# Optimization experiments

Hardware: AMD Instinct MI355X
Metric: run time of the kernel (lower is better)

Reference implementation:

```python
import jax, jax.numpy as jnp
import numpy as np


def _bilinear_warp(img, flow):
    """grid_sample(img, base_grid + flow), bilinear, zeros padding, align_corners=True.
    img: [N, C, H, W]; flow: [N, 2, H, W] with channels (dx, dy) in pixels."""
    N, C, H, W = img.shape
    ys, xs = jnp.meshgrid(jnp.arange(H, dtype=img.dtype),
                          jnp.arange(W, dtype=img.dtype), indexing='ij')
    x = xs[None] + flow[:, 0]  # [N, H, W] sample x-coord in pixels
    y = ys[None] + flow[:, 1]
    x0 = jnp.floor(x)
    y0 = jnp.floor(y)
    wx1 = x - x0
    wy1 = y - y0

    def tap(xi, yi, w):
        valid = (xi >= 0) & (xi <= W - 1) & (yi >= 0) & (yi <= H - 1)
        xc = jnp.clip(xi, 0, W - 1).astype(jnp.int32)
        yc = jnp.clip(yi, 0, H - 1).astype(jnp.int32)
        # per-image gather: im[:, yy, xx] -> [C, H, W]
        vals = jax.vmap(lambda im, yy, xx: im[:, yy, xx])(img, yc, xc)
        return vals * (w * valid.astype(img.dtype))[:, None]

    return (tap(x0,       y0,       (1.0 - wx1) * (1.0 - wy1)) +
            tap(x0 + 1.0, y0,       wx1         * (1.0 - wy1)) +
            tap(x0,       y0 + 1.0, (1.0 - wx1) * wy1) +
            tap(x0 + 1.0, y0 + 1.0, wx1         * wy1))


def _to_batch(t):
    # [B, C, T, H, W] -> cat(unbind(dim=2), dim=0) -> [T*B, C, H, W]
    B, C, T, H, W = t.shape
    return jnp.moveaxis(t, 2, 0).reshape(T * B, C, H, W)


def setup_inputs() -> dict:
    key = jax.random.key(0)
    k1, k2, k3, k4 = jax.random.split(key, 4)
    B, C, T, H, W = 8, 2, 8, 512, 512
    flow = jax.random.normal(k1, (B, C, T, H, W), dtype=jnp.float32) * 8.0
    flowback = jax.random.normal(k2, (B, C, T, H, W), dtype=jnp.float32) * 8.0
    mask_fw = jax.random.uniform(k3, (B, 1, T, H, W), dtype=jnp.float32)
    mask_bw = jax.random.uniform(k4, (B, 1, T, H, W), dtype=jnp.float32)
    return {"flow": flow, "flowback": flowback, "mask_fw": mask_fw,
            "mask_bw": mask_bw, "num_predicted_frames": 8}


def reference(flow, flowback, mask_fw, mask_bw, num_predicted_frames):
    f = _to_batch(flow)        # [T*B, 2, H, W]
    fb = _to_batch(flowback)
    mf = _to_batch(mask_fw)    # [T*B, 1, H, W]
    mb = _to_batch(mask_bw)
    nextloss = jnp.mean(mf * jnp.abs(_bilinear_warp(fb, f) + f))
    prevloss = jnp.mean(mb * jnp.abs(_bilinear_warp(f, fb) + fb))
    return (prevloss + nextloss) * num_predicted_frames
```

## Files before the change

### kernel.cpp

```cpp
#include <hip/hip_runtime.h>

#define BB 8
#define CC 2
#define TT 8
#define HH 512
#define WW 512
#define HWSZ (HH * WW)
#define TOTAL_ELEMS ((double)(BB * CC * TT) * (double)HWSZ)

__device__ __forceinline__ float2 ld2(const float* __restrict__ p) {
    float2 v;
    __builtin_memcpy(&v, p, sizeof(float2));
    return v;
}

__device__ __forceinline__ void bilin2(const float* __restrict__ c0,
                                       const float* __restrict__ c1,
                                       float sx, float sy,
                                       float& r0, float& r1)
{
    const float x0f = floorf(sx);
    const float y0f = floorf(sy);
    const float wx1 = sx - x0f;
    const float wy1 = sy - y0f;
    const int x0 = (int)x0f;
    const int y0 = (int)y0f;
    const int y1 = y0 + 1;

    const int xl = min(max(x0, 0), WW - 2);
    const float ax = (1.f - wx1) * ((x0 >= 0 && x0 < WW) ? 1.f : 0.f);
    const float bx = wx1 * ((x0 + 1 >= 0 && x0 + 1 < WW) ? 1.f : 0.f);
    const bool lo_is_x0 = (x0 == xl);
    const float wl = lo_is_x0 ? ax : bx;
    const float wr = lo_is_x0 ? bx : ax;

    const float wyA = (1.f - wy1) * ((y0 >= 0 && y0 < HH) ? 1.f : 0.f);
    const float wyB = wy1 * ((y1 >= 0 && y1 < HH) ? 1.f : 0.f);
    const int ycA = min(max(y0, 0), HH - 1);
    const int ycB = min(max(y1, 0), HH - 1);
    const int baseA = ycA * WW + xl;
    const int baseB = ycB * WW + xl;

    const float2 a0 = ld2(c0 + baseA);
    const float2 b0 = ld2(c0 + baseB);
    const float2 a1 = ld2(c1 + baseA);
    const float2 b1 = ld2(c1 + baseB);

    r0 = wyA * (wl * a0.x + wr * a0.y) + wyB * (wl * b0.x + wr * b0.y);
    r1 = wyA * (wl * a1.x + wr * a1.y) + wyB * (wl * b1.x + wr * b1.y);
}

__global__ __launch_bounds__(256, 6) void flow_loss_kernel(
    const float* __restrict__ flow,
    const float* __restrict__ flowback,
    const float* __restrict__ mask_fw,
    const float* __restrict__ mask_bw,
    double* __restrict__ acc)
{
    const int xcd = blockIdx.x & 7;
    const int o   = blockIdx.x >> 3;

    const int g   = o * 256 + threadIdx.x;
    const int pix = g * 4;
    const int xb  = pix & (WW - 1);
    const int y   = pix >> 9;

    float lsum = 0.f;

    for (int sl = 0; sl < 8; ++sl) {
        const int s = xcd * 8 + sl;
        const int b = s >> 3;
        const int t = s & 7;

        const float* f0 = flow     + (b * 16 + t) * HWSZ;
        const float* f1 = f0 + 8 * HWSZ;
        const float* g0 = flowback + (b * 16 + t) * HWSZ;
        const float* g1 = g0 + 8 * HWSZ;
        const float* mfp = mask_fw + s * HWSZ;
        const float* mbp = mask_bw + s * HWSZ;

        const float4 fxv = *(const float4*)(f0 + pix);
        const float4 fyv = *(const float4*)(f1 + pix);
        const float4 gxv = *(const float4*)(g0 + pix);
        const float4 gyv = *(const float4*)(g1 + pix);
        const float4 mfv = *(const float4*)(mfp + pix);
        const float4 mbv = *(const float4*)(mbp + pix);

        const float fxa[4] = {fxv.x, fxv.y, fxv.z, fxv.w};
        const float fya[4] = {fyv.x, fyv.y, fyv.z, fyv.w};
        const float gxa[4] = {gxv.x, gxv.y, gxv.z, gxv.w};
        const float gya[4] = {gyv.x, gyv.y, gyv.z, gyv.w};
        const float mfa[4] = {mfv.x, mfv.y, mfv.z, mfv.w};
        const float mba[4] = {mbv.x, mbv.y, mbv.z, mbv.w};

#pragma unroll
        for (int k = 0; k < 4; ++k) {
            const float xf = (float)(xb + k);
            const float yf = (float)y;
            float wfbx, wfby, wfx, wfy;
            bilin2(g0, g1, xf + fxa[k], yf + fya[k], wfbx, wfby);
            bilin2(f0, f1, xf + gxa[k], yf + gya[k], wfx, wfy);
            lsum += mfa[k] * (fabsf(wfbx + fxa[k]) + fabsf(wfby + fya[k]))
                  + mba[k] * (fabsf(wfx  + gxa[k]) + fabsf(wfy  + gya[k]));
        }
    }

    for (int off = 32; off > 0; off >>= 1)
        lsum += __shfl_down(lsum, off, 64);

    __shared__ float wsum[4];
    const int lane = threadIdx.x & 63;
    const int wv   = threadIdx.x >> 6;
    if (lane == 0) wsum[wv] = lsum;
    __syncthreads();
    if (threadIdx.x == 0) {
        float ssum = wsum[0] + wsum[1] + wsum[2] + wsum[3];
        atomicAdd(acc, (double)ssum);
    }
}

__global__ void finalize_kernel(const double* __restrict__ acc,
                                const int* __restrict__ npf,
                                float* __restrict__ out)
{
    out[0] = (float)(acc[0] * ((double)npf[0] / TOTAL_ELEMS));
}

extern "C" void kernel_launch(void* const* d_in, const int* in_sizes, int n_in,
                              void* d_out, int out_size, void* d_ws, size_t ws_size,
                              hipStream_t stream)
{
    const float* flow     = (const float*)d_in[0];
    const float* flowback = (const float*)d_in[1];
    const float* mask_fw  = (const float*)d_in[2];
    const float* mask_bw  = (const float*)d_in[3];
    const int*   npf      = (const int*)d_in[4];
    float*  out = (float*)d_out;
    double* acc = (double*)d_ws;

    hipMemsetAsync(d_ws, 0, sizeof(double), stream);

    flow_loss_kernel<<<2048, 256, 0, stream>>>(flow, flowback, mask_fw, mask_bw, acc);
    finalize_kernel<<<1, 1, 0, stream>>>(acc, npf, out);
}
```

Baseline: 890.6 us.

## Repack flow planes into interleaved xy layout before bilinear gather

Adds a repack kernel that writes flow and flowback into a workspace with the x and y channels interleaved, so each bilinear tap fetches both channels with one 16-byte load instead of two 8-byte loads from separate planes. This halves the number of gather instructions and spreads the random accesses over fewer cache lines. In exchange, the full flow tensors are read and written an extra time. The new path needs a workspace of about 268 MB and falls back to the old kernel if the workspace is smaller. Occupancy hint raised to 8 for the new kernel.

Measured after the change: 947.9 us. 1.06x slower.

```diff
diff --git a/kernel.cpp b/kernel.cpp
--- a/kernel.cpp
+++ b/kernel.cpp
@@ -1,23 +1,58 @@
 #include <hip/hip_runtime.h>
 
 #define BB 8
-#define CC 2
 #define TT 8
 #define HH 512
 #define WW 512
 #define HWSZ (HH * WW)
-#define TOTAL_ELEMS ((double)(BB * CC * TT) * (double)HWSZ)
+#define NSL  (BB * TT)
+#define TOTAL_ELEMS 33554432.0
+
+#define SLICE_FLOATS (HWSZ * 2)
+#define ACC_OFF      0
+#define FI_OFF       512
+#define GI_OFF       (FI_OFF + (size_t)NSL * SLICE_FLOATS * 4)
+#define WS_NEEDED    (GI_OFF + (size_t)NSL * SLICE_FLOATS * 4)
 
 __device__ __forceinline__ float2 ld2(const float* __restrict__ p) {
-    float2 v;
-    __builtin_memcpy(&v, p, sizeof(float2));
-    return v;
-}
-
-__device__ __forceinline__ void bilin2(const float* __restrict__ c0,
-                                       const float* __restrict__ c1,
-                                       float sx, float sy,
-                                       float& r0, float& r1)
+    float2 v; __builtin_memcpy(&v, p, sizeof(float2)); return v;
+}
+__device__ __forceinline__ float4 ld4u(const float* __restrict__ p) {
+    float4 v; __builtin_memcpy(&v, p, sizeof(float4)); return v;
+}
+
+__global__ __launch_bounds__(256, 8) void repack_kernel(
+    const float* __restrict__ flow,
+    const float* __restrict__ flowback,
+    float* __restrict__ fi,
+    float* __restrict__ gi)
+{
+    const int s = blockIdx.x >> 8;
+    const int o = blockIdx.x & 255;
+    const int b = s >> 3;
+    const int t = s & 7;
+    const int pix = (o * 256 + threadIdx.x) * 4;
+
+    const int ps = (b * 16 + t) * HWSZ;
+    {
+        const float4 c0 = *(const float4*)(flow + ps + pix);
+        const float4 c1 = *(const float4*)(flow + ps + 8 * HWSZ + pix);
+        float* d = fi + (size_t)s * SLICE_FLOATS + 2 * pix;
+        *(float4*)(d)     = make_float4(c0.x, c1.x, c0.y, c1.y);
+        *(float4*)(d + 4) = make_float4(c0.z, c1.z, c0.w, c1.w);
+    }
+    {
+        const float4 c0 = *(const float4*)(flowback + ps + pix);
+        const float4 c1 = *(const float4*)(flowback + ps + 8 * HWSZ + pix);
+        float* d = gi + (size_t)s * SLICE_FLOATS + 2 * pix;
+        *(float4*)(d)     = make_float4(c0.x, c1.x, c0.y, c1.y);
+        *(float4*)(d + 4) = make_float4(c0.z, c1.z, c0.w, c1.w);
+    }
+}
+
+__device__ __forceinline__ void bilin2i(const float* __restrict__ pl,
+                                        float sx, float sy,
+                                        float& r0, float& r1)
 {
     const float x0f = floorf(sx);
     const float y0f = floorf(sy);
@@ -38,28 +73,23 @@
     const float wyB = wy1 * ((y1 >= 0 && y1 < HH) ? 1.f : 0.f);
     const int ycA = min(max(y0, 0), HH - 1);
     const int ycB = min(max(y1, 0), HH - 1);
-    const int baseA = ycA * WW + xl;
-    const int baseB = ycB * WW + xl;
-
-    const float2 a0 = ld2(c0 + baseA);
-    const float2 b0 = ld2(c0 + baseB);
-    const float2 a1 = ld2(c1 + baseA);
-    const float2 b1 = ld2(c1 + baseB);
-
-    r0 = wyA * (wl * a0.x + wr * a0.y) + wyB * (wl * b0.x + wr * b0.y);
-    r1 = wyA * (wl * a1.x + wr * a1.y) + wyB * (wl * b1.x + wr * b1.y);
-}
-
-__global__ __launch_bounds__(256, 6) void flow_loss_kernel(
-    const float* __restrict__ flow,
-    const float* __restrict__ flowback,
+
+    const float4 a = ld4u(pl + 2 * (ycA * WW + xl));
+    const float4 b = ld4u(pl + 2 * (ycB * WW + xl));
+
+    r0 = wyA * (wl * a.x + wr * a.z) + wyB * (wl * b.x + wr * b.z);
+    r1 = wyA * (wl * a.y + wr * a.w) + wyB * (wl * b.y + wr * b.w);
+}
+
+__global__ __launch_bounds__(256, 8) void flow_loss_i_kernel(
+    const float* __restrict__ fi,
+    const float* __restrict__ gi,
     const float* __restrict__ mask_fw,
     const float* __restrict__ mask_bw,
     double* __restrict__ acc)
 {
     const int xcd = blockIdx.x & 7;
     const int o   = blockIdx.x >> 3;
-
     const int g   = o * 256 + threadIdx.x;
     const int pix = g * 4;
     const int xb  = pix & (WW - 1);
@@ -69,27 +99,22 @@
 
     for (int sl = 0; sl < 8; ++sl) {
         const int s = xcd * 8 + sl;
-        const int b = s >> 3;
-        const int t = s & 7;
-
-        const float* f0 = flow     + (b * 16 + t) * HWSZ;
-        const float* f1 = f0 + 8 * HWSZ;
-        const float* g0 = flowback + (b * 16 + t) * HWSZ;
-        const float* g1 = g0 + 8 * HWSZ;
-        const float* mfp = mask_fw + s * HWSZ;
-        const float* mbp = mask_bw + s * HWSZ;
-
-        const float4 fxv = *(const float4*)(f0 + pix);
-        const float4 fyv = *(const float4*)(f1 + pix);
-        const float4 gxv = *(const float4*)(g0 + pix);
-        const float4 gyv = *(const float4*)(g1 + pix);
+        const float* fp = fi + (size_t)s * SLICE_FLOATS;
+        const float* gp = gi + (size_t)s * SLICE_FLOATS;
+        const float* mfp = mask_fw + (size_t)s * HWSZ;
+        const float* mbp = mask_bw + (size_t)s * HWSZ;
+
+        const float4 f01 = *(const float4*)(fp + 2 * pix);
+        const float4 f23 = *(const float4*)(fp + 2 * pix + 4);
+        const float4 g01 = *(const float4*)(gp + 2 * pix);
+        const float4 g23 = *(const float4*)(gp + 2 * pix + 4);
         const float4 mfv = *(const float4*)(mfp + pix);
         const float4 mbv = *(const float4*)(mbp + pix);
 
-        const float fxa[4] = {fxv.x, fxv.y, fxv.z, fxv.w};
-        const float fya[4] = {fyv.x, fyv.y, fyv.z, fyv.w};
-        const float gxa[4] = {gxv.x, gxv.y, gxv.z, gxv.w};
-        const float gya[4] = {gyv.x, gyv.y, gyv.z, gyv.w};
+        const float fxa[4] = {f01.x, f01.z, f23.x, f23.z};
+        const float fya[4] = {f01.y, f01.w, f23.y, f23.w};
+        const float gxa[4] = {g01.x, g01.z, g23.x, g23.z};
+        const float gya[4] = {g01.y, g01.w, g23.y, g23.w};
         const float mfa[4] = {mfv.x, mfv.y, mfv.z, mfv.w};
         const float mba[4] = {mbv.x, mbv.y, mbv.z, mbv.w};
 
@@ -98,8 +123,8 @@
             const float xf = (float)(xb + k);
             const float yf = (float)y;
             float wfbx, wfby, wfx, wfy;
-            bilin2(g0, g1, xf + fxa[k], yf + fya[k], wfbx, wfby);
-            bilin2(f0, f1, xf + gxa[k], yf + gya[k], wfx, wfy);
+            bilin2i(gp, xf + fxa[k], yf + fya[k], wfbx, wfby);
+            bilin2i(fp, xf + gxa[k], yf + gya[k], wfx, wfy);
             lsum += mfa[k] * (fabsf(wfbx + fxa[k]) + fabsf(wfby + fya[k]))
                   + mba[k] * (fabsf(wfx  + gxa[k]) + fabsf(wfy  + gya[k]));
         }
@@ -119,6 +144,96 @@
     }
 }
 
+__device__ __forceinline__ void bilin2p(const float* __restrict__ c0,
+                                        const float* __restrict__ c1,
+                                        float sx, float sy,
+                                        float& r0, float& r1)
+{
+    const float x0f = floorf(sx);
+    const float y0f = floorf(sy);
+    const float wx1 = sx - x0f;
+    const float wy1 = sy - y0f;
+    const int x0 = (int)x0f;
+    const int y0 = (int)y0f;
+    const int y1 = y0 + 1;
+    const int xl = min(max(x0, 0), WW - 2);
+    const float ax = (1.f - wx1) * ((x0 >= 0 && x0 < WW) ? 1.f : 0.f);
+    const float bx = wx1 * ((x0 + 1 >= 0 && x0 + 1 < WW) ? 1.f : 0.f);
+    const bool lo_is_x0 = (x0 == xl);
+    const float wl = lo_is_x0 ? ax : bx;
+    const float wr = lo_is_x0 ? bx : ax;
+    const float wyA = (1.f - wy1) * ((y0 >= 0 && y0 < HH) ? 1.f : 0.f);
+    const float wyB = wy1 * ((y1 >= 0 && y1 < HH) ? 1.f : 0.f);
+    const int baseA = (min(max(y0, 0), HH - 1)) * WW + xl;
+    const int baseB = (min(max(y1, 0), HH - 1)) * WW + xl;
+    const float2 a0 = ld2(c0 + baseA);
+    const float2 b0 = ld2(c0 + baseB);
+    const float2 a1 = ld2(c1 + baseA);
+    const float2 b1 = ld2(c1 + baseB);
+    r0 = wyA * (wl * a0.x + wr * a0.y) + wyB * (wl * b0.x + wr * b0.y);
+    r1 = wyA * (wl * a1.x + wr * a1.y) + wyB * (wl * b1.x + wr * b1.y);
+}
+
+__global__ __launch_bounds__(256, 6) void flow_loss_p_kernel(
+    const float* __restrict__ flow,
+    const float* __restrict__ flowback,
+    const float* __restrict__ mask_fw,
+    const float* __restrict__ mask_bw,
+    double* __restrict__ acc)
+{
+    const int xcd = blockIdx.x & 7;
+    const int o   = blockIdx.x >> 3;
+    const int g   = o * 256 + threadIdx.x;
+    const int pix = g * 4;
+    const int xb  = pix & (WW - 1);
+    const int y   = pix >> 9;
+    float lsum = 0.f;
+    for (int sl = 0; sl < 8; ++sl) {
+        const int s = xcd * 8 + sl;
+        const int b = s >> 3;
+        const int t = s & 7;
+        const float* f0 = flow     + (b * 16 + t) * HWSZ;
+        const float* f1 = f0 + 8 * HWSZ;
+        const float* g0 = flowback + (b * 16 + t) * HWSZ;
+        const float* g1 = g0 + 8 * HWSZ;
+        const float* mfp = mask_fw + s * HWSZ;
+        const float* mbp = mask_bw + s * HWSZ;
+        const float4 fxv = *(const float4*)(f0 + pix);
+        const float4 fyv = *(const float4*)(f1 + pix);
+        const float4 gxv = *(const float4*)(g0 + pix);
+        const float4 gyv = *(const float4*)(g1 + pix);
+        const float4 mfv = *(const float4*)(mfp + pix);
+        const float4 mbv = *(const float4*)(mbp + pix);
+        const float fxa[4] = {fxv.x, fxv.y, fxv.z, fxv.w};
+        const float fya[4] = {fyv.x, fyv.y, fyv.z, fyv.w};
+        const float gxa[4] = {gxv.x, gxv.y, gxv.z, gxv.w};
+        const float gya[4] = {gyv.x, gyv.y, gyv.z, gyv.w};
+        const float mfa[4] = {mfv.x, mfv.y, mfv.z, mfv.w};
+        const float mba[4] = {mbv.x, mbv.y, mbv.z, mbv.w};
+#pragma unroll
+        for (int k = 0; k < 4; ++k) {
+            const float xf = (float)(xb + k);
+            const float yf = (float)y;
+            float wfbx, wfby, wfx, wfy;
+            bilin2p(g0, g1, xf + fxa[k], yf + fya[k], wfbx, wfby);
+            bilin2p(f0, f1, xf + gxa[k], yf + gya[k], wfx, wfy);
+            lsum += mfa[k] * (fabsf(wfbx + fxa[k]) + fabsf(wfby + fya[k]))
+                  + mba[k] * (fabsf(wfx  + gxa[k]) + fabsf(wfy  + gya[k]));
+        }
+    }
+    for (int off = 32; off > 0; off >>= 1)
+        lsum += __shfl_down(lsum, off, 64);
+    __shared__ float wsum[4];
+    const int lane = threadIdx.x & 63;
+    const int wv   = threadIdx.x >> 6;
+    if (lane == 0) wsum[wv] = lsum;
+    __syncthreads();
+    if (threadIdx.x == 0) {
+        float ssum = wsum[0] + wsum[1] + wsum[2] + wsum[3];
+        atomicAdd(acc, (double)ssum);
+    }
+}
+
 __global__ void finalize_kernel(const double* __restrict__ acc,
                                 const int* __restrict__ npf,
                                 float* __restrict__ out)
@@ -140,6 +255,13 @@
 
     hipMemsetAsync(d_ws, 0, sizeof(double), stream);
 
-    flow_loss_kernel<<<2048, 256, 0, stream>>>(flow, flowback, mask_fw, mask_bw, acc);
+    if (ws_size >= WS_NEEDED) {
+        float* fi = (float*)((char*)d_ws + FI_OFF);
+        float* gi = (float*)((char*)d_ws + GI_OFF);
+        repack_kernel<<<NSL * 256, 256, 0, stream>>>(flow, flowback, fi, gi);
+        flow_loss_i_kernel<<<2048, 256, 0, stream>>>(fi, gi, mask_fw, mask_bw, acc);
+    } else {
+        flow_loss_p_kernel<<<2048, 256, 0, stream>>>(flow, flowback, mask_fw, mask_bw, acc);
+    }
     finalize_kernel<<<1, 1, 0, stream>>>(acc, npf, out);
 }
```
